# Kernel tuning notes

Measured on AMD Instinct MI355X. Metric: run time of the kernel, lower is better.

## Reference

```python
import jax, jax.numpy as jnp
import numpy as np

NUM_LAYERS = 3
BUFFER_SIZE = 5
RECENCY = 0.9
LOW_POWER_K = 8

B, N, S, C = 8, 8192, 64, 16


def setup_inputs() -> dict:
    key = jax.random.key(0)
    ks = jax.random.split(key, 8)
    return {
        "x": jax.random.normal(ks[0], (B, N, S), jnp.float32),
        "entanglement": jax.random.normal(ks[1], (N, S), jnp.float32),
        # mixing initialized as identity in the module; perturb slightly so it is non-trivial
        "mixing": jnp.eye(N, dtype=jnp.float32) + 0.01 * jax.random.normal(ks[2], (N, N), jnp.float32),
        "readout_w": jax.random.normal(ks[3], (S, S), jnp.float32) / np.sqrt(S).astype(np.float32),
        "enc_w": jax.random.normal(ks[4], (C, S), jnp.float32) / np.sqrt(S).astype(np.float32),
        "enc_b": jnp.zeros((C,), jnp.float32),
        "dec_w": jax.random.normal(ks[5], (S, C), jnp.float32) / np.sqrt(C).astype(np.float32),
        "dec_b": jnp.zeros((S,), jnp.float32),
    }


def _temporal_proximity_scaling(stack, recency_factor):
    # stack: [T, N, S] of buffered activations, stack[-1] most recent.
    # Recency-weighted mean: most recent weight 1, older decayed by recency_factor.
    T = stack.shape[0]
    w = recency_factor ** jnp.arange(T - 1, -1, -1, dtype=stack.dtype)  # [T]
    return jnp.einsum('t,tns->ns', w, stack) / jnp.sum(w)


def _low_power_collapse(s, k):
    # keep top-k |values| per neuron row, zero the rest
    a = jnp.abs(s)
    vals, _ = jax.lax.top_k(a, k)           # [N, k]
    thr = vals[:, -1:]                       # kth largest magnitude per row
    return jnp.where(a >= thr, s, jnp.zeros_like(s))


def reference(x, entanglement, mixing, readout_w, enc_w, enc_b, dec_w, dec_b):
    gate = jax.nn.sigmoid(entanglement)[None]  # [1, N, S]
    buf = []  # ShortTermBuffer contents, vectorized over all neurons: list of [N, S]
    ns = jnp.zeros((N, S), x.dtype)
    for _ in range(NUM_LAYERS):
        # NOTE: the torch code prunes/decays/resets neuron_states at the top of each
        # layer but immediately overwrites it with x.mean(0) -> dead code, omitted.
        x = x * gate
        x = jnp.einsum('bns,nm->bms', x, mixing)
        ns = jnp.mean(x, axis=0)  # [N, S]
        buf.append(ns)
        buf = buf[-BUFFER_SIZE:]
        stack = jnp.stack(buf, axis=0)        # [T, N, S], T = min(layer+1, BUFFER_SIZE)
        ns = _temporal_proximity_scaling(stack, RECENCY)
        # advanced_state_collapse via autoencoder (importance_threshold=0.0 -> always reconstruct)
        h = jax.nn.relu(ns @ enc_w.T + enc_b)  # [N, C]
        ns = h @ dec_w.T + dec_b               # [N, S]
        ns = _low_power_collapse(ns, LOW_POWER_K)
    out = x @ readout_w.T  # Linear(S, S, bias=False)
    # torch forward returns only readout(x); neuron_states is a mutated buffer.
    # We also return it so the memory-bound per-neuron state pipeline is not DCE'd.
    return out, ns
```

## Files before the change

kernel.cpp:

```cpp
#include <hip/hip_runtime.h>

#define NN 8192
#define SS 64
#define BSD 512
#define NS (NN*SS)
#define NBS (NN*BSD)

typedef __attribute__((ext_vector_type(4))) _Float16 f16x4;
typedef __attribute__((ext_vector_type(8))) _Float16 f16x8;
typedef __attribute__((ext_vector_type(4))) float f32x4;

#define GLOAD_LDS16(gptr, lptr) \
    __builtin_amdgcn_global_load_lds((const __attribute__((address_space(1))) void*)(gptr), \
                                     (__attribute__((address_space(3))) void*)(lptr), 16, 0, 0)

__device__ __forceinline__ int kmap(int lane, int e) {
    return ((lane >> 4) << 2) + (e & 3) + ((e >> 2) << 4);
}

__global__ void sigmoid_gate_kernel(const float* __restrict__ ent, float* __restrict__ gate) {
    int i = blockIdx.x * 256 + threadIdx.x;
    gate[i] = 1.0f / (1.0f + expf(-ent[i]));
}

__global__ __launch_bounds__(256) void convA_kernel(const float* __restrict__ Mx,
                                                    char* __restrict__ Ab) {
    __shared__ _Float16 Lh[64][136];
    __shared__ _Float16 Ll[64][136];
    const int t = threadIdx.x;
    const int kt = blockIdx.x, mt = blockIdx.y;
    const int k0 = kt * 64, m0 = mt * 128;
    #pragma unroll
    for (int i = 0; i < 8; ++i) {
        int e = i * 256 + t;
        int kr = e >> 5, m4 = (e & 31) << 2;
        float4 v = *(const float4*)&Mx[(size_t)(k0 + kr) * NN + m0 + m4];
        int d = (k0 + kr) - (m0 + m4);
        if (d == 0) v.x -= 1.0f;
        if (d == 1) v.y -= 1.0f;
        if (d == 2) v.z -= 1.0f;
        if (d == 3) v.w -= 1.0f;
        f16x4 h, l;
        h[0] = (_Float16)v.x; l[0] = (_Float16)(v.x - (float)h[0]);
        h[1] = (_Float16)v.y; l[1] = (_Float16)(v.y - (float)h[1]);
        h[2] = (_Float16)v.z; l[2] = (_Float16)(v.z - (float)h[2]);
        h[3] = (_Float16)v.w; l[3] = (_Float16)(v.w - (float)h[3]);
        *(f16x4*)&Lh[kr][m4] = h;
        *(f16x4*)&Ll[kr][m4] = l;
    }
    __syncthreads();
    #pragma unroll
    for (int j = 0; j < 4; ++j) {
        int idx  = j * 256 + t;
        int h    = idx >> 9;
        int w    = idx & 511;
        int blk  = w >> 7;
        int kk   = (w >> 6) & 1;
        int lane = w & 63;
        int col  = h * 64 + blk * 16 + (lane & 15);
        int kb   = kk * 32;
        f16x8 hv, lv;
        #pragma unroll
        for (int e = 0; e < 8; ++e) {
            int k = kb + kmap(lane, e);
            hv[e] = Lh[k][col];
            lv[e] = Ll[k][col];
        }
        char* tile = Ab + (((size_t)(mt * 2 + h) * 128 + kt) << 14);
        *(f16x8*)(tile + w * 16)        = hv;
        *(f16x8*)(tile + 8192 + w * 16) = lv;
    }
}

__device__ __forceinline__ void pack_B(const _Float16 (*Lh)[520],
                                       const _Float16 (*Nh)[72], const _Float16 (*Nl)[72],
                                       char* Bb, char* Nb, int kt, int t) {
    #pragma unroll
    for (int j = 0; j < 16; ++j) {
        int idx = j * 256 + t;
        int nbt = idx >> 10, w = idx & 1023;
        int blk = w >> 7, kk = (w >> 6) & 1, lane = w & 63;
        int col = nbt * 128 + blk * 16 + (lane & 15);
        int kb = kk * 32;
        f16x8 hv;
        #pragma unroll
        for (int e = 0; e < 8; ++e)
            hv[e] = Lh[kb + kmap(lane, e)][col];
        *(f16x8*)(Bb + (((size_t)kt * 4 + nbt) << 14) + w * 16) = hv;
    }
    #pragma unroll
    for (int j = 0; j < 4; ++j) {
        int idx = j * 256 + t;
        int nbt = idx >> 8, r = idx & 255;
        int part = r >> 7, kk = (r >> 6) & 1, lane = r & 63;
        int s = nbt * 16 + (lane & 15);
        int kb = kk * 32;
        f16x8 v;
        #pragma unroll
        for (int e = 0; e < 8; ++e) {
            int k = kb + kmap(lane, e);
            v[e] = part ? Nl[k][s] : Nh[k][s];
        }
        *(f16x8*)(Nb + (((size_t)kt * 4 + nbt) << 12) + part * 2048 + kk * 1024 + lane * 16) = v;
    }
}

__global__ __launch_bounds__(256) void prep0_kernel(const float* __restrict__ x,
                                                    const float* __restrict__ gate,
                                                    float* __restrict__ X,
                                                    char* __restrict__ Bb,
                                                    char* __restrict__ Nb,
                                                    float* __restrict__ mg32) {
    __shared__ _Float16 Lh[64][520];
    __shared__ _Float16 Nh[64][72];
    __shared__ _Float16 Nl[64][72];
    const int t = threadIdx.x;
    const int kt = blockIdx.x;
    const int n0 = kt * 64;
    #pragma unroll
    for (int i = 0; i < 4; ++i) {
        int e = i * 256 + t;
        int kr = e >> 4;
        int s4 = (e & 15) << 2;
        float4 g = *(const float4*)&gate[(size_t)(n0 + kr) * 64 + s4];
        float4 ms = make_float4(0.f, 0.f, 0.f, 0.f);
        #pragma unroll
        for (int b = 0; b < 8; ++b) {
            float4 v = *(const float4*)&x[((size_t)b * NN + n0 + kr) * 64 + s4];
            ms.x += v.x; ms.y += v.y; ms.z += v.z; ms.w += v.w;
            v.x *= g.x; v.y *= g.y; v.z *= g.z; v.w *= g.w;
            *(float4*)&X[(size_t)(n0 + kr) * BSD + b * 64 + s4] = v;
            f16x4 h;
            h[0] = (_Float16)v.x; h[1] = (_Float16)v.y;
            h[2] = (_Float16)v.z; h[3] = (_Float16)v.w;
            *(f16x4*)&Lh[kr][b * 64 + s4] = h;
        }
        float4 mg4;
        mg4.x = ms.x * 0.125f * g.x; mg4.y = ms.y * 0.125f * g.y;
        mg4.z = ms.z * 0.125f * g.z; mg4.w = ms.w * 0.125f * g.w;
        *(float4*)&mg32[(size_t)(n0 + kr) * 64 + s4] = mg4;
        f16x4 mh, ml;
        mh[0] = (_Float16)mg4.x; ml[0] = (_Float16)(mg4.x - (float)mh[0]);
        mh[1] = (_Float16)mg4.y; ml[1] = (_Float16)(mg4.y - (float)mh[1]);
        mh[2] = (_Float16)mg4.z; ml[2] = (_Float16)(mg4.z - (float)mh[2]);
        mh[3] = (_Float16)mg4.w; ml[3] = (_Float16)(mg4.w - (float)mh[3]);
        *(f16x4*)&Nh[kr][s4] = mh;
        *(f16x4*)&Nl[kr][s4] = ml;
    }
    __syncthreads();
    pack_B(Lh, Nh, Nl, Bb, Nb, kt, t);
}

__global__ __launch_bounds__(256) void gateconv_kernel(float* __restrict__ X,
                                                       const float* __restrict__ gate,
                                                       const float* __restrict__ nsprev,
                                                       char* __restrict__ Bb,
                                                       char* __restrict__ Nb,
                                                       float* __restrict__ mg32) {
    __shared__ _Float16 Lh[64][520];
    __shared__ _Float16 Nh[64][72];
    __shared__ _Float16 Nl[64][72];
    const int t = threadIdx.x;
    const int kt = blockIdx.x;
    const int n0 = kt * 64;
    #pragma unroll
    for (int i = 0; i < 32; ++i) {
        int e = i * 256 + t;
        int kr = e >> 7;
        int c4 = (e & 127) << 2;
        float4 v = *(const float4*)&X[(size_t)(n0 + kr) * BSD + c4];
        float4 g = *(const float4*)&gate[(size_t)(n0 + kr) * 64 + (c4 & 63)];
        v.x *= g.x; v.y *= g.y; v.z *= g.z; v.w *= g.w;
        *(float4*)&X[(size_t)(n0 + kr) * BSD + c4] = v;
        f16x4 h;
        h[0] = (_Float16)v.x; h[1] = (_Float16)v.y;
        h[2] = (_Float16)v.z; h[3] = (_Float16)v.w;
        *(f16x4*)&Lh[kr][c4] = h;
    }
    #pragma unroll
    for (int i = 0; i < 4; ++i) {
        int e = i * 256 + t;
        int kr = e >> 4;
        int s4 = (e & 15) << 2;
        float4 p = *(const float4*)&nsprev[(size_t)(n0 + kr) * 64 + s4];
        float4 g = *(const float4*)&gate[(size_t)(n0 + kr) * 64 + s4];
        float4 mg4;
        mg4.x = p.x * g.x; mg4.y = p.y * g.y; mg4.z = p.z * g.z; mg4.w = p.w * g.w;
        *(float4*)&mg32[(size_t)(n0 + kr) * 64 + s4] = mg4;
        f16x4 mh, ml;
        mh[0] = (_Float16)mg4.x; ml[0] = (_Float16)(mg4.x - (float)mh[0]);
        mh[1] = (_Float16)mg4.y; ml[1] = (_Float16)(mg4.y - (float)mh[1]);
        mh[2] = (_Float16)mg4.z; ml[2] = (_Float16)(mg4.z - (float)mh[2]);
        mh[3] = (_Float16)mg4.w; ml[3] = (_Float16)(mg4.w - (float)mh[3]);
        *(f16x4*)&Nh[kr][s4] = mh;
        *(f16x4*)&Nl[kr][s4] = ml;
    }
    __syncthreads();
    pack_B(Lh, Nh, Nl, Bb, Nb, kt, t);
}

__global__ __launch_bounds__(256) void gemm_f16_kernel(const char* __restrict__ Ab,
                                                       const char* __restrict__ Bb,
                                                       const char* __restrict__ Nb,
                                                       float* X,
                                                       const float* __restrict__ mg,
                                                       float* __restrict__ nsout) {
    __shared__ char lds[2][36864];
    const int t = threadIdx.x;
    const int L = blockIdx.x;
    const int mt  = (L & 7) + ((L >> 5) << 3);
    const int nbt = (L >> 3) & 3;
    const int lane = t & 63, wid = t >> 6;

    const char* gA = Ab + (((size_t)mt * 128) << 14) + wid * 2048 + lane * 16;
    const char* gB = Bb + (((size_t)nbt) << 14) + wid * 4096 + lane * 16;
    const char* gN = Nb + (((size_t)nbt) << 12) + wid * 1024 + lane * 16;
    const uint32_t lA = wid * 2048;
    const uint32_t lB = 16384 + wid * 4096;
    const uint32_t lN = 32768 + wid * 1024;

    auto stage = [&](char* la, const char* pA, const char* pB, const char* pN) {
        GLOAD_LDS16(pA,               la + lA);
        GLOAD_LDS16(pA + 1024,        la + lA + 1024);
        GLOAD_LDS16(pA + 8192,        la + lA + 8192);
        GLOAD_LDS16(pA + 8192 + 1024, la + lA + 8192 + 1024);
        GLOAD_LDS16(pB,               la + lB);
        GLOAD_LDS16(pB + 1024,        la + lB + 1024);
        GLOAD_LDS16(pB + 2048,        la + lB + 2048);
        GLOAD_LDS16(pB + 3072,        la + lB + 3072);
        GLOAD_LDS16(pN,               la + lN);
    };

    f32x4 accm[4][2];
    #pragma unroll
    for (int fi = 0; fi < 4; ++fi) {
        accm[fi][0] = (f32x4){0.f, 0.f, 0.f, 0.f};
        accm[fi][1] = (f32x4){0.f, 0.f, 0.f, 0.f};
    }
    f32x4 accn = (f32x4){0.f, 0.f, 0.f, 0.f};

    stage(lds[0], gA, gB, gN);
    gA += 16384; gB += 65536; gN += 16384;

    for (int kt = 0; kt < 128; ++kt) {
        const int cur = kt & 1;
        asm volatile("s_waitcnt vmcnt(0)" ::: "memory");
        __builtin_amdgcn_s_barrier();
        __builtin_amdgcn_sched_barrier(0);
        if (kt < 127) {
            stage(lds[cur ^ 1], gA, gB, gN);
            gA += 16384; gB += 65536; gN += 16384;
        }
        __builtin_amdgcn_sched_barrier(0);
        const char* base = lds[cur];
        const char* A_ = base + lane * 16;
        const char* Bm = base + 16384 + wid * 4096 + lane * 16;
        const char* Bn = base + 32768 + lane * 16;
        #pragma unroll
        for (int kk = 0; kk < 2; ++kk) {
            const int ko = kk * 1024;
            f16x8 bm0 = *(const f16x8*)(Bm + ko);
            f16x8 bm1 = *(const f16x8*)(Bm + 2048 + ko);
            f16x8 bnh = *(const f16x8*)(Bn + ko);
            f16x8 bnl = *(const f16x8*)(Bn + 2048 + ko);
            #pragma unroll
            for (int fi = 0; fi < 4; ++fi) {
                f16x8 ah = *(const f16x8*)(A_ + fi * 2048 + ko);
                accm[fi][0] = __builtin_amdgcn_mfma_f32_16x16x32_f16(ah, bm0, accm[fi][0], 0, 0, 0);
                accm[fi][1] = __builtin_amdgcn_mfma_f32_16x16x32_f16(ah, bm1, accm[fi][1], 0, 0, 0);
                if (fi == wid) {
                    f16x8 aln = *(const f16x8*)(A_ + 8192 + fi * 2048 + ko);
                    accn = __builtin_amdgcn_mfma_f32_16x16x32_f16(ah,  bnh, accn, 0, 0, 0);
                    accn = __builtin_amdgcn_mfma_f32_16x16x32_f16(ah,  bnl, accn, 0, 0, 0);
                    accn = __builtin_amdgcn_mfma_f32_16x16x32_f16(aln, bnh, accn, 0, 0, 0);
                }
            }
        }
    }

    const int row0 = mt * 64 + ((lane >> 4) << 2);
    const int col0 = nbt * 128 + wid * 32 + (lane & 15);
    #pragma unroll
    for (int fi = 0; fi < 4; ++fi)
        #pragma unroll
        for (int fj = 0; fj < 2; ++fj)
            #pragma unroll
            for (int j = 0; j < 4; ++j) {
                size_t idx = (size_t)(row0 + fi * 16 + j) * BSD + col0 + fj * 16;
                X[idx] = accm[fi][fj][j] + X[idx];
            }
    const int nr0 = mt * 64 + wid * 16 + ((lane >> 4) << 2);
    const int nc  = nbt * 16 + (lane & 15);
    #pragma unroll
    for (int j = 0; j < 4; ++j) {
        size_t nidx = (size_t)(nr0 + j) * 64 + nc;
        nsout[nidx] = accn[j] + mg[nidx];
    }
}

__global__ __launch_bounds__(256) void readout_kernel(const float* __restrict__ X3,
                                                      const float* __restrict__ W,
                                                      float* __restrict__ out) {
    __shared__ float Wt[64][65];
    __shared__ float xr[512];
    const int n = blockIdx.x;
    const int t = threadIdx.x;
    for (int e = t; e < 4096; e += 256) {
        int s = e >> 6, sp = e & 63;
        Wt[sp][s] = W[e];
    }
    xr[t]       = X3[(size_t)n * BSD + t];
    xr[t + 256] = X3[(size_t)n * BSD + 256 + t];
    __syncthreads();
    const int b1 = t >> 6;
    const int s  = t & 63;
    float acc0 = 0.0f, acc1 = 0.0f;
    #pragma unroll
    for (int sp = 0; sp < 64; ++sp) {
        float w = Wt[sp][s];
        acc0 += w * xr[b1 * 64 + sp];
        acc1 += w * xr[(b1 + 4) * 64 + sp];
    }
    out[((size_t)b1 * NN + n) * SS + s]       = acc0;
    out[((size_t)(b1 + 4) * NN + n) * SS + s] = acc1;
}

__global__ void nsfinal_kernel(const float* __restrict__ ns0,
                               const float* __restrict__ enc_w, const float* __restrict__ enc_b,
                               const float* __restrict__ dec_w, const float* __restrict__ dec_b,
                               float* __restrict__ out_ns) {
    int gtid = blockIdx.x * 256 + threadIdx.x;
    int lane = gtid & 63;
    const float r = 0.9f;
    const float wsum = 1.0f + r + r * r;
    float tns = (ns0[gtid] * (r * r) + ns0[NS + gtid] * r + ns0[2 * NS + gtid]) / wsum;
    float v = dec_b[lane];
    #pragma unroll
    for (int c = 0; c < 16; ++c) {
        float p = tns * enc_w[c * 64 + lane];
        #pragma unroll
        for (int off = 32; off; off >>= 1) p += __shfl_xor(p, off, 64);
        float h = fmaxf(p + enc_b[c], 0.0f);
        v += h * dec_w[lane * 16 + c];
    }
    float av = fabsf(v);
    int cnt = 0;
    for (int j = 0; j < 64; ++j) {
        float o = __shfl(av, j, 64);
        cnt += (o > av) ? 1 : 0;
    }
    out_ns[gtid] = (cnt < 8) ? v : 0.0f;
}

extern "C" void kernel_launch(void* const* d_in, const int* in_sizes, int n_in,
                              void* d_out, int out_size, void* d_ws, size_t ws_size,
                              hipStream_t stream) {
    const float* x      = (const float*)d_in[0];
    const float* ent    = (const float*)d_in[1];
    const float* mixing = (const float*)d_in[2];
    const float* r_w    = (const float*)d_in[3];
    const float* enc_w  = (const float*)d_in[4];
    const float* enc_b  = (const float*)d_in[5];
    const float* dec_w  = (const float*)d_in[6];
    const float* dec_b  = (const float*)d_in[7];
    float* out = (float*)d_out;

    char*  Ab   = (char*)d_ws;
    char*  Bb   = Ab + 268435456ull;
    char*  Nb   = Bb + 8388608ull;
    float* X    = (float*)(Nb + 2097152ull);
    float* mg32 = X + NBS;
    float* ns0  = mg32 + NS;
    float* gate = ns0 + 3 * (size_t)NS;

    sigmoid_gate_kernel<<<NS / 256, 256, 0, stream>>>(ent, gate);
    convA_kernel<<<dim3(128, 64), 256, 0, stream>>>(mixing, Ab);
    prep0_kernel<<<128, 256, 0, stream>>>(x, gate, X, Bb, Nb, mg32);

    for (int l = 0; l < 3; ++l) {
        gemm_f16_kernel<<<512, 256, 0, stream>>>(Ab, Bb, Nb, X, mg32, ns0 + (size_t)l * NS);
        if (l < 2)
            gateconv_kernel<<<128, 256, 0, stream>>>(X, gate, ns0 + (size_t)l * NS, Bb, Nb, mg32);
    }

    readout_kernel<<<NN, 256, 0, stream>>>(X, r_w, out);
    nsfinal_kernel<<<2048, 256, 0, stream>>>(ns0, enc_w, enc_b, dec_w, dec_b, out + NBS);
}
```

Before: 683.0 us.

## Triple-buffer A in LDS and load B operands directly into registers

The GEMM main loop moves from a double-buffered LDS pipeline with a full vmcnt(0) wait to a three-stage pipeline. Only the A tile is staged through LDS; the B and N fragments are loaded straight from global memory into per-stage register arrays, and the wait becomes vmcnt(12) so one stage's loads stay in flight. The LDS footprint drops and launch bounds request two blocks per CU, which is meant to hide memory latency. The cost is higher register pressure from the 24 buffered f16x8 values, and the register-load layout of B and N must exactly match the old LDS reads.

```diff
diff --git a/kernel.cpp b/kernel.cpp
--- a/kernel.cpp
+++ b/kernel.cpp
@@ -199,13 +199,13 @@
     pack_B(Lh, Nh, Nl, Bb, Nb, kt, t);
 }
 
-__global__ __launch_bounds__(256) void gemm_f16_kernel(const char* __restrict__ Ab,
-                                                       const char* __restrict__ Bb,
-                                                       const char* __restrict__ Nb,
-                                                       float* X,
-                                                       const float* __restrict__ mg,
-                                                       float* __restrict__ nsout) {
-    __shared__ char lds[2][36864];
+__global__ __launch_bounds__(256, 2) void gemm_f16_kernel(const char* __restrict__ Ab,
+                                                          const char* __restrict__ Bb,
+                                                          const char* __restrict__ Nb,
+                                                          float* X,
+                                                          const float* __restrict__ mg,
+                                                          float* __restrict__ nsout) {
+    __shared__ char lds[3][16384];
     const int t = threadIdx.x;
     const int L = blockIdx.x;
     const int mt  = (L & 7) + ((L >> 5) << 3);
@@ -214,21 +214,25 @@
 
     const char* gA = Ab + (((size_t)mt * 128) << 14) + wid * 2048 + lane * 16;
     const char* gB = Bb + (((size_t)nbt) << 14) + wid * 4096 + lane * 16;
-    const char* gN = Nb + (((size_t)nbt) << 12) + wid * 1024 + lane * 16;
+    const char* gN = Nb + (((size_t)nbt) << 12) + lane * 16;
     const uint32_t lA = wid * 2048;
-    const uint32_t lB = 16384 + wid * 4096;
-    const uint32_t lN = 32768 + wid * 1024;
-
-    auto stage = [&](char* la, const char* pA, const char* pB, const char* pN) {
-        GLOAD_LDS16(pA,               la + lA);
-        GLOAD_LDS16(pA + 1024,        la + lA + 1024);
-        GLOAD_LDS16(pA + 8192,        la + lA + 8192);
-        GLOAD_LDS16(pA + 8192 + 1024, la + lA + 8192 + 1024);
-        GLOAD_LDS16(pB,               la + lB);
-        GLOAD_LDS16(pB + 1024,        la + lB + 1024);
-        GLOAD_LDS16(pB + 2048,        la + lB + 2048);
-        GLOAD_LDS16(pB + 3072,        la + lB + 3072);
-        GLOAD_LDS16(pN,               la + lN);
+
+    f16x8 B0[4], B1[4], B2[4], N0[4], N1[4], N2[4];
+
+    auto stage = [&](char* la, f16x8* Br, f16x8* Nr) {
+        GLOAD_LDS16(gA,               la + lA);
+        GLOAD_LDS16(gA + 1024,        la + lA + 1024);
+        GLOAD_LDS16(gA + 8192,        la + lA + 8192);
+        GLOAD_LDS16(gA + 8192 + 1024, la + lA + 8192 + 1024);
+        Br[0] = *(const f16x8*)(gB);
+        Br[1] = *(const f16x8*)(gB + 1024);
+        Br[2] = *(const f16x8*)(gB + 2048);
+        Br[3] = *(const f16x8*)(gB + 3072);
+        Nr[0] = *(const f16x8*)(gN);
+        Nr[1] = *(const f16x8*)(gN + 1024);
+        Nr[2] = *(const f16x8*)(gN + 2048);
+        Nr[3] = *(const f16x8*)(gN + 3072);
+        gA += 16384; gB += 65536; gN += 16384;
     };
 
     f32x4 accm[4][2];
@@ -239,44 +243,51 @@
     }
     f32x4 accn = (f32x4){0.f, 0.f, 0.f, 0.f};
 
-    stage(lds[0], gA, gB, gN);
-    gA += 16384; gB += 65536; gN += 16384;
-
-    for (int kt = 0; kt < 128; ++kt) {
-        const int cur = kt & 1;
-        asm volatile("s_waitcnt vmcnt(0)" ::: "memory");
-        __builtin_amdgcn_s_barrier();
-        __builtin_amdgcn_sched_barrier(0);
-        if (kt < 127) {
-            stage(lds[cur ^ 1], gA, gB, gN);
-            gA += 16384; gB += 65536; gN += 16384;
-        }
-        __builtin_amdgcn_sched_barrier(0);
-        const char* base = lds[cur];
+    auto compute = [&](const char* base, const f16x8* Br, const f16x8* Nr) {
         const char* A_ = base + lane * 16;
-        const char* Bm = base + 16384 + wid * 4096 + lane * 16;
-        const char* Bn = base + 32768 + lane * 16;
         #pragma unroll
         for (int kk = 0; kk < 2; ++kk) {
             const int ko = kk * 1024;
-            f16x8 bm0 = *(const f16x8*)(Bm + ko);
-            f16x8 bm1 = *(const f16x8*)(Bm + 2048 + ko);
-            f16x8 bnh = *(const f16x8*)(Bn + ko);
-            f16x8 bnl = *(const f16x8*)(Bn + 2048 + ko);
             #pragma unroll
             for (int fi = 0; fi < 4; ++fi) {
                 f16x8 ah = *(const f16x8*)(A_ + fi * 2048 + ko);
-                accm[fi][0] = __builtin_amdgcn_mfma_f32_16x16x32_f16(ah, bm0, accm[fi][0], 0, 0, 0);
-                accm[fi][1] = __builtin_amdgcn_mfma_f32_16x16x32_f16(ah, bm1, accm[fi][1], 0, 0, 0);
+                accm[fi][0] = __builtin_amdgcn_mfma_f32_16x16x32_f16(ah, Br[kk],     accm[fi][0], 0, 0, 0);
+                accm[fi][1] = __builtin_amdgcn_mfma_f32_16x16x32_f16(ah, Br[2 + kk], accm[fi][1], 0, 0, 0);
                 if (fi == wid) {
                     f16x8 aln = *(const f16x8*)(A_ + 8192 + fi * 2048 + ko);
-                    accn = __builtin_amdgcn_mfma_f32_16x16x32_f16(ah,  bnh, accn, 0, 0, 0);
-                    accn = __builtin_amdgcn_mfma_f32_16x16x32_f16(ah,  bnl, accn, 0, 0, 0);
-                    accn = __builtin_amdgcn_mfma_f32_16x16x32_f16(aln, bnh, accn, 0, 0, 0);
+                    accn = __builtin_amdgcn_mfma_f32_16x16x32_f16(ah,  Nr[kk],     accn, 0, 0, 0);
+                    accn = __builtin_amdgcn_mfma_f32_16x16x32_f16(ah,  Nr[2 + kk], accn, 0, 0, 0);
+                    accn = __builtin_amdgcn_mfma_f32_16x16x32_f16(aln, Nr[kk],     accn, 0, 0, 0);
                 }
             }
         }
-    }
+    };
+
+#define PIPE_STEP(CURSLOT, BC, NC, PFSLOT, BP, NP)                      \
+    asm volatile("s_waitcnt vmcnt(12)" ::: "memory");                   \
+    __builtin_amdgcn_s_barrier();                                       \
+    __builtin_amdgcn_sched_barrier(0);                                  \
+    stage(lds[PFSLOT], BP, NP);                                         \
+    __builtin_amdgcn_sched_barrier(0);                                  \
+    compute(lds[CURSLOT], BC, NC);
+
+    stage(lds[0], B0, N0);
+    stage(lds[1], B1, N1);
+    #pragma unroll 1
+    for (int it = 0; it < 42; ++it) {
+        PIPE_STEP(0, B0, N0, 2, B2, N2)
+        PIPE_STEP(1, B1, N1, 0, B0, N0)
+        PIPE_STEP(2, B2, N2, 1, B1, N1)
+    }
+    asm volatile("s_waitcnt vmcnt(12)" ::: "memory");
+    __builtin_amdgcn_s_barrier();
+    __builtin_amdgcn_sched_barrier(0);
+    compute(lds[0], B0, N0);
+    asm volatile("s_waitcnt vmcnt(0)" ::: "memory");
+    __builtin_amdgcn_s_barrier();
+    __builtin_amdgcn_sched_barrier(0);
+    compute(lds[1], B1, N1);
+#undef PIPE_STEP
 
     const int row0 = mt * 64 + ((lane >> 4) << 2);
     const int col0 = nbt * 128 + wid * 32 + (lane & 15);
```

Result: slower. 759.4 us (+11.2%).

## Load B operand directly to registers and double K-step per stage

Applied to the files above, without the earlier changes.

The GEMM main loop now stages two K-tiles of A and N per LDS buffer, while the B operand is loaded straight from global memory into registers instead of going through LDS. A partial vmcnt wait lets the next stage's loads stay in flight while the current buffer is computed, and the occupancy hint is raised to two blocks per CU. The aim is to cut LDS traffic and barrier frequency and to overlap memory with MFMA work. In exchange it uses many more VGPRs for the B register buffers, and the hand-counted vmcnt values could become wrong if the compiler reorders or splits loads.

```diff
diff --git a/kernel.cpp b/kernel.cpp
--- a/kernel.cpp
+++ b/kernel.cpp
@@ -199,13 +199,13 @@
     pack_B(Lh, Nh, Nl, Bb, Nb, kt, t);
 }
 
-__global__ __launch_bounds__(256) void gemm_f16_kernel(const char* __restrict__ Ab,
-                                                       const char* __restrict__ Bb,
-                                                       const char* __restrict__ Nb,
-                                                       float* X,
-                                                       const float* __restrict__ mg,
-                                                       float* __restrict__ nsout) {
-    __shared__ char lds[2][36864];
+__global__ __launch_bounds__(256, 2) void gemm_f16_kernel(const char* __restrict__ Ab,
+                                                          const char* __restrict__ Bb,
+                                                          const char* __restrict__ Nb,
+                                                          float* X,
+                                                          const float* __restrict__ mg,
+                                                          float* __restrict__ nsout) {
+    __shared__ char lds[2][40960];
     const int t = threadIdx.x;
     const int L = blockIdx.x;
     const int mt  = (L & 7) + ((L >> 5) << 3);
@@ -216,19 +216,30 @@
     const char* gB = Bb + (((size_t)nbt) << 14) + wid * 4096 + lane * 16;
     const char* gN = Nb + (((size_t)nbt) << 12) + wid * 1024 + lane * 16;
     const uint32_t lA = wid * 2048;
-    const uint32_t lB = 16384 + wid * 4096;
     const uint32_t lN = 32768 + wid * 1024;
 
-    auto stage = [&](char* la, const char* pA, const char* pB, const char* pN) {
-        GLOAD_LDS16(pA,               la + lA);
-        GLOAD_LDS16(pA + 1024,        la + lA + 1024);
-        GLOAD_LDS16(pA + 8192,        la + lA + 8192);
-        GLOAD_LDS16(pA + 8192 + 1024, la + lA + 8192 + 1024);
-        GLOAD_LDS16(pB,               la + lB);
-        GLOAD_LDS16(pB + 1024,        la + lB + 1024);
-        GLOAD_LDS16(pB + 2048,        la + lB + 2048);
-        GLOAD_LDS16(pB + 3072,        la + lB + 3072);
-        GLOAD_LDS16(pN,               la + lN);
+    f16x8 B0[8], B1[8];
+
+    auto stage = [&](char* la, f16x8* Br) {
+        GLOAD_LDS16(gA,                       la + lA);
+        GLOAD_LDS16(gA + 1024,                la + lA + 1024);
+        GLOAD_LDS16(gA + 8192,                la + lA + 8192);
+        GLOAD_LDS16(gA + 8192 + 1024,         la + lA + 8192 + 1024);
+        GLOAD_LDS16(gA + 16384,               la + 16384 + lA);
+        GLOAD_LDS16(gA + 16384 + 1024,        la + 16384 + lA + 1024);
+        GLOAD_LDS16(gA + 16384 + 8192,        la + 16384 + lA + 8192);
+        GLOAD_LDS16(gA + 16384 + 8192 + 1024, la + 16384 + lA + 8192 + 1024);
+        GLOAD_LDS16(gN,                       la + lN);
+        GLOAD_LDS16(gN + 16384,               la + lN + 4096);
+        Br[0] = *(const f16x8*)(gB);
+        Br[1] = *(const f16x8*)(gB + 1024);
+        Br[2] = *(const f16x8*)(gB + 2048);
+        Br[3] = *(const f16x8*)(gB + 3072);
+        Br[4] = *(const f16x8*)(gB + 65536);
+        Br[5] = *(const f16x8*)(gB + 65536 + 1024);
+        Br[6] = *(const f16x8*)(gB + 65536 + 2048);
+        Br[7] = *(const f16x8*)(gB + 65536 + 3072);
+        gA += 32768; gB += 131072; gN += 32768;
     };
 
     f32x4 accm[4][2];
@@ -239,43 +250,47 @@
     }
     f32x4 accn = (f32x4){0.f, 0.f, 0.f, 0.f};
 
-    stage(lds[0], gA, gB, gN);
-    gA += 16384; gB += 65536; gN += 16384;
-
-    for (int kt = 0; kt < 128; ++kt) {
-        const int cur = kt & 1;
-        asm volatile("s_waitcnt vmcnt(0)" ::: "memory");
-        __builtin_amdgcn_s_barrier();
-        __builtin_amdgcn_sched_barrier(0);
-        if (kt < 127) {
-            stage(lds[cur ^ 1], gA, gB, gN);
-            gA += 16384; gB += 65536; gN += 16384;
-        }
-        __builtin_amdgcn_sched_barrier(0);
-        const char* base = lds[cur];
+    auto compute = [&](const char* base, const f16x8* Br) {
         const char* A_ = base + lane * 16;
-        const char* Bm = base + 16384 + wid * 4096 + lane * 16;
-        const char* Bn = base + 32768 + lane * 16;
-        #pragma unroll
-        for (int kk = 0; kk < 2; ++kk) {
-            const int ko = kk * 1024;
-            f16x8 bm0 = *(const f16x8*)(Bm + ko);
-            f16x8 bm1 = *(const f16x8*)(Bm + 2048 + ko);
-            f16x8 bnh = *(const f16x8*)(Bn + ko);
-            f16x8 bnl = *(const f16x8*)(Bn + 2048 + ko);
+        const char* N_ = base + 32768 + lane * 16;
+        #pragma unroll
+        for (int kk = 0; kk < 4; ++kk) {
+            const int ao = (kk >> 1) * 16384 + (kk & 1) * 1024;
+            const int no = (kk >> 1) * 4096 + (kk & 1) * 1024;
+            const int bi = (kk >> 1) * 4 + (kk & 1);
+            f16x8 bnh = *(const f16x8*)(N_ + no);
+            f16x8 bnl = *(const f16x8*)(N_ + no + 2048);
             #pragma unroll
             for (int fi = 0; fi < 4; ++fi) {
-                f16x8 ah = *(const f16x8*)(A_ + fi * 2048 + ko);
-                accm[fi][0] = __builtin_amdgcn_mfma_f32_16x16x32_f16(ah, bm0, accm[fi][0], 0, 0, 0);
-                accm[fi][1] = __builtin_amdgcn_mfma_f32_16x16x32_f16(ah, bm1, accm[fi][1], 0, 0, 0);
+                f16x8 ah = *(const f16x8*)(A_ + ao + fi * 2048);
+                accm[fi][0] = __builtin_amdgcn_mfma_f32_16x16x32_f16(ah, Br[bi],     accm[fi][0], 0, 0, 0);
+                accm[fi][1] = __builtin_amdgcn_mfma_f32_16x16x32_f16(ah, Br[bi + 2], accm[fi][1], 0, 0, 0);
                 if (fi == wid) {
-                    f16x8 aln = *(const f16x8*)(A_ + 8192 + fi * 2048 + ko);
+                    f16x8 aln = *(const f16x8*)(A_ + ao + 8192 + fi * 2048);
                     accn = __builtin_amdgcn_mfma_f32_16x16x32_f16(ah,  bnh, accn, 0, 0, 0);
                     accn = __builtin_amdgcn_mfma_f32_16x16x32_f16(ah,  bnl, accn, 0, 0, 0);
                     accn = __builtin_amdgcn_mfma_f32_16x16x32_f16(aln, bnh, accn, 0, 0, 0);
                 }
             }
         }
+    };
+
+    stage(lds[0], B0);
+    for (int u = 0; u < 32; ++u) {
+        stage(lds[1], B1);
+        asm volatile("s_waitcnt vmcnt(18)" ::: "memory");
+        __builtin_amdgcn_s_barrier();
+        compute(lds[0], B0);
+        __builtin_amdgcn_s_barrier();
+        if (u < 31) {
+            stage(lds[0], B0);
+            asm volatile("s_waitcnt vmcnt(18)" ::: "memory");
+        } else {
+            asm volatile("s_waitcnt vmcnt(0)" ::: "memory");
+        }
+        __builtin_amdgcn_s_barrier();
+        compute(lds[1], B1);
+        __builtin_amdgcn_s_barrier();
     }
 
     const int row0 = mt * 64 + ((lane >> 4) << 2);
```

Result: no change. 682.6 us (-0.1%).
